# Performance work log

Hardware: AMD Instinct MI355X
Metric: run time of the kernel (lower is better)

The kernel has to match this reference:

```python
import jax, jax.numpy as jnp
import numpy as np
from jax.scipy.special import logsumexp

C = 21; H = 512; W = 512
THETA_ALPHA = 160.0; THETA_BETA = 3.0; THETA_GAMMA = 3.0
NUM_ITER = 5; RADIUS = 7  # truncated gaussian radius for the filter surrogate


def _gauss_kernel(sigma, radius=RADIUS):
    x = jnp.arange(-radius, radius + 1, dtype=jnp.float32)
    k = jnp.exp(-0.5 * (x / sigma) ** 2)
    return k / jnp.sum(k)


def _blur(x, sigma):
    # x: (c, h, w) -> depthwise separable gaussian blur, SAME padding
    c = x.shape[0]
    k = _gauss_kernel(sigma)
    kh = jnp.tile(k.reshape(1, 1, -1, 1), (c, 1, 1, 1))
    kw = jnp.tile(k.reshape(1, 1, 1, -1), (c, 1, 1, 1))
    y = jax.lax.conv_general_dilated(x[None], kh, (1, 1), 'SAME', feature_group_count=c)
    y = jax.lax.conv_general_dilated(y, kw, (1, 1), 'SAME', feature_group_count=c)
    return y[0]


def _high_dim_filter(x, rgb, bilateral):
    # Differentiable surrogate for the external permutohedral high_dim_filter op.
    if bilateral:
        # range weight from rgb (normalized to [0,1]); spatial sigma ~ theta_alpha
        guide = jnp.exp(-0.5 * jnp.sum((rgb / 255.0) ** 2, axis=0, keepdims=True) / (THETA_BETA ** 2))
        return _blur(x * guide, THETA_ALPHA / 16.0)
    return _blur(x, THETA_GAMMA)


def _combined_update(q, low_w, high_w, sp_map, sp_idx):
    # q: (c,h,w), sp_map: (h,w) int, sp_idx: scalar int
    condb = (sp_map[None] == sp_idx)                      # (1,h,w) bool
    cond = condb.astype(q.dtype)
    bool_max = (q == jnp.max(q, axis=0, keepdims=True))   # (c,h,w)
    qc = cond * q                                         # q_val_for_clique
    maxlab = jnp.max(qc, axis=0, keepdims=True)           # (1,h,w)
    l_eq = jnp.where(bool_max & condb, q, 0.0)            # l_prime_equals_l
    A_np = qc + maxlab - l_eq                             # A_no_padding
    q_sum_t = A_np                                        # single clique per iter
    prod_sp = cond * logsumexp(qc, axis=(1, 2))[:, None, None]
    prod_io = cond * logsumexp(A_np, axis=(1, 2))[:, None, None]  # cond^2 == cond
    cond2 = (sp_map[None] == sp_idx + 1).astype(q.dtype)
    prod_att = prod_sp + cond2 * logsumexp(cond2 * q, axis=(1, 2))[:, None, None]
    q_mod = q + (q == 0).astype(q.dtype)
    q_sum_t = q_sum_t + (q_sum_t == 0).astype(q.dtype)

    def upd(prod, denom, lw, hw):
        ft = prod / denom
        return lw[:, None, None] * ft + hw * (1.0 - ft)

    return (upd(prod_sp, q_mod, low_w[0], high_w[0])
            + upd(prod_io, q_sum_t, low_w[1], high_w[1])
            + upd(prod_att, q_mod, low_w[2], high_w[2]))


def setup_inputs() -> dict:
    key = jax.random.key(0)
    k1, k2, k3, k4 = jax.random.split(key, 4)
    unaries = jax.random.normal(k1, (1, H, W, C), dtype=jnp.float32)
    rgb = jax.random.uniform(k2, (1, H, W, 3), dtype=jnp.float32) * 255.0
    sp_map = jax.random.randint(k3, (1, H, W), 0, 500, dtype=jnp.int32)
    sp_indices = jax.random.randint(k4, (NUM_ITER,), 200, 400, dtype=jnp.int32)
    return {
        'unaries': unaries,
        'rgb': rgb,
        'sp_map': sp_map,
        'sp_indices': sp_indices,
        'spatial_ker_weights': jnp.eye(C, dtype=jnp.float32),
        'bilateral_ker_weights': jnp.eye(C, dtype=jnp.float32),
        'complex_rel_low_weights': jnp.ones((3, C), dtype=jnp.float32),
        'complex_rel_high_weights': jnp.ones((3,), dtype=jnp.float32),
        'compatibility_matrix': -jnp.eye(C, dtype=jnp.float32),
    }


def reference(unaries, rgb, sp_map, sp_indices, spatial_ker_weights,
              bilateral_ker_weights, complex_rel_low_weights,
              complex_rel_high_weights, compatibility_matrix):
    u = jnp.transpose(unaries[0], (2, 0, 1))   # (c,h,w)
    im = jnp.transpose(rgb[0], (2, 0, 1))      # (3,h,w)
    spm = jnp.transpose(sp_map[0])             # (h,w), matches tf.transpose
    ones = jnp.ones((C, H, W), dtype=jnp.float32)
    spatial_norm = _high_dim_filter(ones, im, False)
    bilateral_norm = _high_dim_filter(ones, im, True)
    q = u
    for i in range(NUM_ITER):
        sm = jax.nn.softmax(q, axis=0)
        spatial_out = _high_dim_filter(sm, im, False) / spatial_norm
        bilateral_out = _high_dim_filter(sm, im, True) / bilateral_norm
        cru = _combined_update(q, complex_rel_low_weights, complex_rel_high_weights,
                               spm, sp_indices[i])
        mp = (spatial_ker_weights @ spatial_out.reshape(C, -1)
              + bilateral_ker_weights @ bilateral_out.reshape(C, -1))
        pairwise = (compatibility_matrix @ mp).reshape(C, H, W)
        q = u - pairwise - cru
    return jnp.transpose(q, (1, 2, 0))[None]  # (1,h,w,c)
```

## Files before the change

### kernel.cpp

```cpp
#include <hip/hip_runtime.h>
#include <math.h>

#define CC 21
#define HH 512
#define WW 512
#define HWN (HH*WW)
#define CHW (CC*HWN)
#define RAD 7
#define KS 15
#define NITER 5
#define NBKT 16

#define TW 128
#define TH 16
#define TWH (TW + 2*RAD)
#define LSTR 145

#define FEXP(x) __expf(x)
#define FLOG(x) __logf(x)
#define FRCP(x) __builtin_amdgcn_rcpf(x)

__global__ void k_init_small(const float* __restrict__ cm,
                             const float* __restrict__ skw,
                             const float* __restrict__ bkw,
                             float* __restrict__ M1t, float* __restrict__ M2t,
                             float* __restrict__ d1, float* __restrict__ d2,
                             int* __restrict__ dflag,
                             float* __restrict__ kbuf,
                             float* __restrict__ sums) {
    __shared__ int sbad;
    int t = threadIdx.x;
    if (t == 0) sbad = 0;
    __syncthreads();
    if (t < CC*CC) {
        int k = t / CC, c = t % CC;
        float a = 0.f, b = 0.f;
        for (int m = 0; m < CC; ++m) {
            a += cm[c*CC+m] * skw[m*CC+k];
            b += cm[c*CC+m] * bkw[m*CC+k];
        }
        M1t[t] = a; M2t[t] = b;
        if (k != c && (a != 0.f || b != 0.f)) atomicOr(&sbad, 1);
        if (k == c) { d1[c] = a; d2[c] = b; }
    }
    for (int i = t; i < NITER*NBKT*64; i += blockDim.x) sums[i] = 0.f;
    if (t == CC*CC) {
        float w3[KS], w10[KS];
        float s3 = 0.f, s10 = 0.f;
        for (int i = 0; i < KS; ++i) {
            float x = (float)(i - RAD);
            w3[i]  = expf(-0.5f * (x/3.0f)  * (x/3.0f));
            w10[i] = expf(-0.5f * (x/10.0f) * (x/10.0f));
            s3 += w3[i]; s10 += w10[i];
        }
        for (int i = 0; i < KS; ++i) {
            kbuf[i]      = w3[i]  / s3;
            kbuf[KS + i] = w10[i] / s10;
        }
    }
    __syncthreads();
    if (t == 0) dflag[0] = sbad ? 0 : 1;
}

__global__ void k_init_maps(const float* __restrict__ rgb,
                            const int* __restrict__ spin,
                            const float* __restrict__ un,
                            float* __restrict__ guide,
                            int* __restrict__ spmT,
                            float* __restrict__ sm,
                            const int* __restrict__ spidx,
                            float* __restrict__ sums0) {
    int p = blockIdx.x * blockDim.x + threadIdx.x;
    int h = p / WW, w = p - h*WW;
    float r = rgb[p*3+0] * (1.0f/255.0f);
    float g = rgb[p*3+1] * (1.0f/255.0f);
    float b = rgb[p*3+2] * (1.0f/255.0f);
    guide[p] = FEXP(-0.5f * (r*r + g*g + b*b) / 9.0f);
    int s = spin[w*HH + h];
    spmT[p] = s;
    float v[CC];
    #pragma unroll
    for (int c = 0; c < CC; ++c) v[c] = un[p*CC + c];
    float mx = v[0];
    #pragma unroll
    for (int c = 1; c < CC; ++c) mx = fmaxf(mx, v[c]);
    float e[CC], ssum = 0.f;
    #pragma unroll
    for (int c = 0; c < CC; ++c) { e[c] = FEXP(v[c] - mx); ssum += e[c]; }
    float inv = FRCP(ssum);
    #pragma unroll
    for (int c = 0; c < CC; ++c) sm[c*HWN + p] = e[c] * inv;

    int sidx = spidx[0];
    bool c1 = (s == sidx), c2 = (s == sidx + 1);
    if (c1 || c2) {
        float* bkt = sums0 + (blockIdx.x & (NBKT-1)) * 64;
        float emx = FEXP(mx);
        if (c1) {
            #pragma unroll
            for (int c = 0; c < CC; ++c) {
                float ev = e[c] * emx;
                atomicAdd(&bkt[c], ev - 1.0f);
                float ea = (v[c] == mx) ? emx : ev * emx;
                atomicAdd(&bkt[CC + c], ea - 1.0f);
            }
        } else {
            #pragma unroll
            for (int c = 0; c < CC; ++c) atomicAdd(&bkt[2*CC + c], e[c] * emx - 1.0f);
        }
    }
}

__global__ void __launch_bounds__(256, 4)
k_blur(const float* __restrict__ in,
       const float* __restrict__ guide,
       float* __restrict__ outs, float* __restrict__ outb,
       const float* __restrict__ rsn, const float* __restrict__ rbn,
       const float* __restrict__ d1, const float* __restrict__ d2,
       const int* __restrict__ dflag,
       const float* __restrict__ kbuf, int norm_mode) {
    __shared__ float vbs[TH][LSTR];
    __shared__ float vbb[TH][LSTR];
    __shared__ float k3s[KS], k10s[KS];
    int t = threadIdx.x;
    if (t < KS) { k3s[t] = kbuf[t]; k10s[t] = kbuf[KS + t]; }
    __syncthreads();

    int c  = blockIdx.z;
    int x0 = blockIdx.x * TW;
    int y0 = blockIdx.y * TH;
    const float* base = in ? (in + (size_t)c*HWN) : nullptr;

    for (int u = t; u < 2*TWH; u += 256) {
        int col  = (u < TWH) ? u : u - TWH;
        int half = (u < TWH) ? 0 : 1;
        int xg = x0 - RAD + col;
        bool xok = (xg >= 0 && xg < WW);
        int yb = y0 + half*8;
        float ws_[KS], wb_[KS];
        #pragma unroll
        for (int i = 0; i < KS-1; ++i) {
            int yg = yb - RAD + i;
            bool ok = xok && (yg >= 0) && (yg < HH);
            float v = 0.f, g = 0.f;
            if (ok) { g = guide[yg*WW + xg]; v = base ? base[yg*WW + xg] : 1.0f; }
            ws_[i] = v; wb_[i] = v * g;
        }
        #pragma unroll
        for (int y = 0; y < 8; ++y) {
            int yg = yb + y + RAD;
            bool ok = xok && (yg < HH);
            float v = 0.f, g = 0.f;
            if (ok) { g = guide[yg*WW + xg]; v = base ? base[yg*WW + xg] : 1.0f; }
            ws_[(KS-1+y)%KS] = v; wb_[(KS-1+y)%KS] = v * g;
            float as = 0.f, ab = 0.f;
            #pragma unroll
            for (int d = 0; d < KS; ++d) {
                as += k3s[d]  * ws_[(y+d)%KS];
                ab += k10s[d] * wb_[(y+d)%KS];
            }
            vbs[half*8 + y][col] = as; vbb[half*8 + y][col] = ab;
        }
    }
    __syncthreads();

    int oy = t & 15;
    int xs = (t >> 4) * 8;
    int gy = y0 + oy;
    int rowp = gy*WW + x0 + xs;
    size_t ob = (size_t)c*HWN + rowp;

    float wS[22], wB[22];
    #pragma unroll
    for (int i = 0; i < 22; ++i) { wS[i] = vbs[oy][xs + i]; wB[i] = vbb[oy][xs + i]; }

    float resS[8], resB[8];
    #pragma unroll
    for (int j = 0; j < 8; ++j) {
        float a = 0.f, b = 0.f;
        #pragma unroll
        for (int d = 0; d < KS; ++d) { a += k3s[d] * wS[j + d]; b += k10s[d] * wB[j + d]; }
        resS[j] = a; resB[j] = b;
    }

    if (norm_mode) {
        #pragma unroll
        for (int j = 0; j < 8; ++j) {
            outs[rowp + j] = 1.0f / resS[j];
            outb[rowp + j] = 1.0f / resB[j];
        }
    } else if (dflag[0]) {
        float d1c = d1[c], d2c = d2[c];
        #pragma unroll
        for (int j = 0; j < 8; ++j)
            outs[ob + j] = d1c * resS[j] * rsn[rowp + j]
                         + d2c * resB[j] * rbn[rowp + j];
    } else {
        #pragma unroll
        for (int j = 0; j < 8; ++j) {
            outs[ob + j] = resS[j] * rsn[rowp + j];
            outb[ob + j] = resB[j] * rbn[rowp + j];
        }
    }
}

__global__ void __launch_bounds__(256, 4)
k_update(const float* __restrict__ un,
         const float* __restrict__ qin,
         const float* __restrict__ pw,
         const float* __restrict__ blo,
         const float* __restrict__ M1t,
         const float* __restrict__ M2t,
         const int* __restrict__ dflag,
         const float* __restrict__ sums_cur,
         float* __restrict__ sums_next,
         const float* __restrict__ lwg,
         const float* __restrict__ hwg,
         const int* __restrict__ spmT,
         const int* __restrict__ spidx, int iter,
         float* __restrict__ q,
         float* __restrict__ sm,
         float* __restrict__ out, int last) {
    __shared__ float slse[3*CC];
    if (threadIdx.x < 3*CC) {
        float s = 0.f;
        #pragma unroll
        for (int b = 0; b < NBKT; ++b) s += sums_cur[b*64 + threadIdx.x];
        slse[threadIdx.x] = FLOG((float)HWN + s);
    }
    __syncthreads();

    int p = blockIdx.x * blockDim.x + threadIdx.x;
    int sidx = spidx[iter];
    int s = spmT[p];
    float f1 = (s == sidx)     ? 1.f : 0.f;
    float f2 = (s == sidx + 1) ? 1.f : 0.f;

    float acc[CC];
    if (dflag[0]) {
        #pragma unroll
        for (int c = 0; c < CC; ++c) acc[c] = pw[c*HWN + p];
    } else {
        #pragma unroll
        for (int c = 0; c < CC; ++c) acc[c] = 0.f;
        #pragma unroll
        for (int k = 0; k < CC; ++k) {
            float sv = pw[k*HWN + p];
            float bv = blo[k*HWN + p];
            #pragma unroll
            for (int c = 0; c < CC; ++c)
                acc[c] += M1t[k*CC + c] * sv + M2t[k*CC + c] * bv;
        }
    }

    float hw0 = hwg[0], hw1 = hwg[1], hw2 = hwg[2];
    bool any_clique = __any(f1 != 0.f || f2 != 0.f);
    if (any_clique) {
        float v[CC];
        #pragma unroll
        for (int c = 0; c < CC; ++c) v[c] = qin[p*CC + c];
        float mx = v[0];
        #pragma unroll
        for (int c = 1; c < CC; ++c) mx = fmaxf(mx, v[c]);
        #pragma unroll
        for (int c = 0; c < CC; ++c) {
            float qv = v[c];
            float qmod = qv + ((qv == 0.f) ? 1.f : 0.f);
            float anp = f1 * (qv + mx) - ((f1 != 0.f && qv == mx) ? qv : 0.f);
            float qst = anp + ((anp == 0.f) ? 1.f : 0.f);
            float p1 = f1 * slse[c];
            float p2 = f1 * slse[CC + c];
            float p3 = p1 + f2 * slse[2*CC + c];
            float ft1 = p1 * FRCP(qmod);
            float ft2 = p2 * FRCP(qst);
            float ft3 = p3 * FRCP(qmod);
            float cru = lwg[c]*ft1        + hw0*(1.f - ft1)
                      + lwg[CC + c]*ft2   + hw1*(1.f - ft2)
                      + lwg[2*CC + c]*ft3 + hw2*(1.f - ft3);
            acc[c] = un[p*CC + c] - acc[c] - cru;
        }
    } else {
        float cruc = hw0 + hw1 + hw2;
        #pragma unroll
        for (int c = 0; c < CC; ++c)
            acc[c] = un[p*CC + c] - acc[c] - cruc;
    }

    if (!last) {
        int sidx2 = spidx[iter + 1];
        bool c1 = (s == sidx2), c2 = (s == sidx2 + 1);
        if (c1 || c2) {
            #pragma unroll
            for (int c = 0; c < CC; ++c) q[p*CC + c] = acc[c];
        }
        float mx2 = acc[0];
        #pragma unroll
        for (int c = 1; c < CC; ++c) mx2 = fmaxf(mx2, acc[c]);
        float e[CC], ssum = 0.f;
        #pragma unroll
        for (int c = 0; c < CC; ++c) { e[c] = FEXP(acc[c] - mx2); ssum += e[c]; }
        float inv = FRCP(ssum);
        #pragma unroll
        for (int c = 0; c < CC; ++c) sm[c*HWN + p] = e[c] * inv;

        if (c1 || c2) {
            float* bkt = sums_next + (blockIdx.x & (NBKT-1)) * 64;
            float emx = FEXP(mx2);
            if (c1) {
                #pragma unroll
                for (int c = 0; c < CC; ++c) {
                    float ev = e[c] * emx;
                    atomicAdd(&bkt[c], ev - 1.0f);
                    float ea = (acc[c] == mx2) ? emx : ev * emx;
                    atomicAdd(&bkt[CC + c], ea - 1.0f);
                }
            } else {
                #pragma unroll
                for (int c = 0; c < CC; ++c) atomicAdd(&bkt[2*CC + c], e[c] * emx - 1.0f);
            }
        }
    } else {
        #pragma unroll
        for (int c = 0; c < CC; ++c) out[p*CC + c] = acc[c];
    }
}

extern "C" void kernel_launch(void* const* d_in, const int* in_sizes, int n_in,
                              void* d_out, int out_size, void* d_ws, size_t ws_size,
                              hipStream_t stream) {
    const float* un    = (const float*)d_in[0];
    const float* rgb   = (const float*)d_in[1];
    const int*   spin  = (const int*)  d_in[2];
    const int*   spidx = (const int*)  d_in[3];
    const float* skw   = (const float*)d_in[4];
    const float* bkw   = (const float*)d_in[5];
    const float* lw    = (const float*)d_in[6];
    const float* hwv   = (const float*)d_in[7];
    const float* cm    = (const float*)d_in[8];
    float* out = (float*)d_out;

    float* ws = (float*)d_ws;
    float* q     = ws;
    float* sm    = ws + (size_t)CHW;
    float* a     = ws + (size_t)2*CHW;
    float* b     = ws + (size_t)3*CHW;
    float* guide = ws + (size_t)4*CHW;
    float* rsn   = guide + HWN;
    float* rbn   = rsn + HWN;
    int*   spmT  = (int*)(rbn + HWN);
    float* M1t   = rbn + 2*(size_t)HWN;
    float* M2t   = M1t + CC*CC;
    float* d1    = M2t + CC*CC;
    float* d2    = d1 + CC;
    int*   dflag = (int*)(d2 + CC);
    float* kbuf  = d2 + CC + 4;
    float* sums  = kbuf + 2*KS;

    dim3 blk(256);
    int gpix = HWN / 256;
    dim3 gblur(WW/TW, HH/TH, CC);
    dim3 gnorm(WW/TW, HH/TH, 1);

    k_init_small<<<1, 512, 0, stream>>>(cm, skw, bkw, M1t, M2t, d1, d2, dflag,
                                        kbuf, sums);
    k_init_maps<<<gpix, blk, 0, stream>>>(rgb, spin, un, guide, spmT, sm,
                                          spidx, sums);
    k_blur<<<gnorm, blk, 0, stream>>>(nullptr, guide, rsn, rbn,
                                      nullptr, nullptr, d1, d2, dflag, kbuf, 1);

    for (int it = 0; it < NITER; ++it) {
        int last = (it == NITER - 1) ? 1 : 0;
        float* su  = sums + it*NBKT*64;
        float* sun = last ? nullptr : (sums + (it+1)*NBKT*64);
        const float* qin = (it == 0) ? un : q;
        k_blur<<<gblur, blk, 0, stream>>>(sm, guide, a, b, rsn, rbn,
                                          d1, d2, dflag, kbuf, 0);
        k_update<<<gpix, blk, 0, stream>>>(un, qin, a, b, M1t, M2t, dflag,
                                           su, sun, lw, hwv,
                                           spmT, spidx, it, q, sm, out, last);
    }
}
```

Before: 343.1 us.

## Store softmax and blur intermediates in bf16 and transpose unaries to planar

Result: slower. 415.2 us (+21.0%).

```diff
diff --git a/kernel.cpp b/kernel.cpp
--- a/kernel.cpp
+++ b/kernel.cpp
@@ -19,6 +19,18 @@
 #define FEXP(x) __expf(x)
 #define FLOG(x) __logf(x)
 #define FRCP(x) __builtin_amdgcn_rcpf(x)
+
+typedef unsigned short ushort_t;
+typedef unsigned int uint_t;
+
+__device__ __forceinline__ float b2f(ushort_t u) {
+    return __uint_as_float(((uint_t)u) << 16);
+}
+__device__ __forceinline__ ushort_t f2b(float f) {
+    uint_t u = __float_as_uint(f);
+    u += 0x7FFFu + ((u >> 16) & 1u);
+    return (ushort_t)(u >> 16);
+}
 
 __global__ void k_init_small(const float* __restrict__ cm,
                              const float* __restrict__ skw,
@@ -67,7 +79,8 @@
                             const float* __restrict__ un,
                             float* __restrict__ guide,
                             int* __restrict__ spmT,
-                            float* __restrict__ sm,
+                            float* __restrict__ unp,
+                            ushort_t* __restrict__ sm,
                             const int* __restrict__ spidx,
                             float* __restrict__ sums0) {
     int p = blockIdx.x * blockDim.x + threadIdx.x;
@@ -80,7 +93,7 @@
     spmT[p] = s;
     float v[CC];
     #pragma unroll
-    for (int c = 0; c < CC; ++c) v[c] = un[p*CC + c];
+    for (int c = 0; c < CC; ++c) { v[c] = un[p*CC + c]; unp[c*HWN + p] = v[c]; }
     float mx = v[0];
     #pragma unroll
     for (int c = 1; c < CC; ++c) mx = fmaxf(mx, v[c]);
@@ -89,7 +102,7 @@
     for (int c = 0; c < CC; ++c) { e[c] = FEXP(v[c] - mx); ssum += e[c]; }
     float inv = FRCP(ssum);
     #pragma unroll
-    for (int c = 0; c < CC; ++c) sm[c*HWN + p] = e[c] * inv;
+    for (int c = 0; c < CC; ++c) sm[c*HWN + p] = f2b(e[c] * inv);
 
     int sidx = spidx[0];
     bool c1 = (s == sidx), c2 = (s == sidx + 1);
@@ -112,13 +125,9 @@
 }
 
 __global__ void __launch_bounds__(256, 4)
-k_blur(const float* __restrict__ in,
-       const float* __restrict__ guide,
-       float* __restrict__ outs, float* __restrict__ outb,
-       const float* __restrict__ rsn, const float* __restrict__ rbn,
-       const float* __restrict__ d1, const float* __restrict__ d2,
-       const int* __restrict__ dflag,
-       const float* __restrict__ kbuf, int norm_mode) {
+k_norm(const float* __restrict__ guide,
+       float* __restrict__ rsn, float* __restrict__ rbn,
+       const float* __restrict__ kbuf) {
     __shared__ float vbs[TH][LSTR];
     __shared__ float vbb[TH][LSTR];
     __shared__ float k3s[KS], k10s[KS];
@@ -126,10 +135,8 @@
     if (t < KS) { k3s[t] = kbuf[t]; k10s[t] = kbuf[KS + t]; }
     __syncthreads();
 
-    int c  = blockIdx.z;
     int x0 = blockIdx.x * TW;
     int y0 = blockIdx.y * TH;
-    const float* base = in ? (in + (size_t)c*HWN) : nullptr;
 
     for (int u = t; u < 2*TWH; u += 256) {
         int col  = (u < TWH) ? u : u - TWH;
@@ -142,17 +149,17 @@
         for (int i = 0; i < KS-1; ++i) {
             int yg = yb - RAD + i;
             bool ok = xok && (yg >= 0) && (yg < HH);
-            float v = 0.f, g = 0.f;
-            if (ok) { g = guide[yg*WW + xg]; v = base ? base[yg*WW + xg] : 1.0f; }
-            ws_[i] = v; wb_[i] = v * g;
+            float v = ok ? 1.0f : 0.f;
+            float g = ok ? guide[yg*WW + xg] : 0.f;
+            ws_[i] = v; wb_[i] = g;
         }
         #pragma unroll
         for (int y = 0; y < 8; ++y) {
             int yg = yb + y + RAD;
             bool ok = xok && (yg < HH);
-            float v = 0.f, g = 0.f;
-            if (ok) { g = guide[yg*WW + xg]; v = base ? base[yg*WW + xg] : 1.0f; }
-            ws_[(KS-1+y)%KS] = v; wb_[(KS-1+y)%KS] = v * g;
+            float v = ok ? 1.0f : 0.f;
+            float g = ok ? guide[yg*WW + xg] : 0.f;
+            ws_[(KS-1+y)%KS] = v; wb_[(KS-1+y)%KS] = g;
             float as = 0.f, ab = 0.f;
             #pragma unroll
             for (int d = 0; d < KS; ++d) {
@@ -166,6 +173,76 @@
 
     int oy = t & 15;
     int xs = (t >> 4) * 8;
+    int rowp = (y0 + oy)*WW + x0 + xs;
+
+    float wS[22], wB[22];
+    #pragma unroll
+    for (int i = 0; i < 22; ++i) { wS[i] = vbs[oy][xs + i]; wB[i] = vbb[oy][xs + i]; }
+    #pragma unroll
+    for (int j = 0; j < 8; ++j) {
+        float a = 0.f, b = 0.f;
+        #pragma unroll
+        for (int d = 0; d < KS; ++d) { a += k3s[d] * wS[j + d]; b += k10s[d] * wB[j + d]; }
+        rsn[rowp + j] = 1.0f / a;
+        rbn[rowp + j] = 1.0f / b;
+    }
+}
+
+__global__ void __launch_bounds__(256, 4)
+k_blur(const ushort_t* __restrict__ in,
+       const float* __restrict__ guide,
+       ushort_t* __restrict__ outs, ushort_t* __restrict__ outb,
+       const float* __restrict__ rsn, const float* __restrict__ rbn,
+       const float* __restrict__ d1, const float* __restrict__ d2,
+       const int* __restrict__ dflag,
+       const float* __restrict__ kbuf) {
+    __shared__ float vbs[TH][LSTR];
+    __shared__ float vbb[TH][LSTR];
+    __shared__ float k3s[KS], k10s[KS];
+    int t = threadIdx.x;
+    if (t < KS) { k3s[t] = kbuf[t]; k10s[t] = kbuf[KS + t]; }
+    __syncthreads();
+
+    int c  = blockIdx.z;
+    int x0 = blockIdx.x * TW;
+    int y0 = blockIdx.y * TH;
+    const ushort_t* base = in + (size_t)c*HWN;
+
+    for (int u = t; u < 2*TWH; u += 256) {
+        int col  = (u < TWH) ? u : u - TWH;
+        int half = (u < TWH) ? 0 : 1;
+        int xg = x0 - RAD + col;
+        bool xok = (xg >= 0 && xg < WW);
+        int yb = y0 + half*8;
+        float ws_[KS], wb_[KS];
+        #pragma unroll
+        for (int i = 0; i < KS-1; ++i) {
+            int yg = yb - RAD + i;
+            bool ok = xok && (yg >= 0) && (yg < HH);
+            float v = 0.f, g = 0.f;
+            if (ok) { g = guide[yg*WW + xg]; v = b2f(base[yg*WW + xg]); }
+            ws_[i] = v; wb_[i] = v * g;
+        }
+        #pragma unroll
+        for (int y = 0; y < 8; ++y) {
+            int yg = yb + y + RAD;
+            bool ok = xok && (yg < HH);
+            float v = 0.f, g = 0.f;
+            if (ok) { g = guide[yg*WW + xg]; v = b2f(base[yg*WW + xg]); }
+            ws_[(KS-1+y)%KS] = v; wb_[(KS-1+y)%KS] = v * g;
+            float as = 0.f, ab = 0.f;
+            #pragma unroll
+            for (int d = 0; d < KS; ++d) {
+                as += k3s[d]  * ws_[(y+d)%KS];
+                ab += k10s[d] * wb_[(y+d)%KS];
+            }
+            vbs[half*8 + y][col] = as; vbb[half*8 + y][col] = ab;
+        }
+    }
+    __syncthreads();
+
+    int oy = t & 15;
+    int xs = (t >> 4) * 8;
     int gy = y0 + oy;
     int rowp = gy*WW + x0 + xs;
     size_t ob = (size_t)c*HWN + rowp;
@@ -183,32 +260,27 @@
         resS[j] = a; resB[j] = b;
     }
 
-    if (norm_mode) {
+    if (dflag[0]) {
+        float d1c = d1[c], d2c = d2[c];
+        #pragma unroll
+        for (int j = 0; j < 8; ++j)
+            outs[ob + j] = f2b(d1c * resS[j] * rsn[rowp + j]
+                             + d2c * resB[j] * rbn[rowp + j]);
+    } else {
         #pragma unroll
         for (int j = 0; j < 8; ++j) {
-            outs[rowp + j] = 1.0f / resS[j];
-            outb[rowp + j] = 1.0f / resB[j];
-        }
-    } else if (dflag[0]) {
-        float d1c = d1[c], d2c = d2[c];
-        #pragma unroll
-        for (int j = 0; j < 8; ++j)
-            outs[ob + j] = d1c * resS[j] * rsn[rowp + j]
-                         + d2c * resB[j] * rbn[rowp + j];
-    } else {
-        #pragma unroll
-        for (int j = 0; j < 8; ++j) {
-            outs[ob + j] = resS[j] * rsn[rowp + j];
-            outb[ob + j] = resB[j] * rbn[rowp + j];
+            outs[ob + j] = f2b(resS[j] * rsn[rowp + j]);
+            outb[ob + j] = f2b(resB[j] * rbn[rowp + j]);
         }
     }
 }
 
 __global__ void __launch_bounds__(256, 4)
-k_update(const float* __restrict__ un,
+k_update(const float* __restrict__ unp,
          const float* __restrict__ qin,
-         const float* __restrict__ pw,
-         const float* __restrict__ blo,
+         int qin_pixelmajor_unused,
+         const ushort_t* __restrict__ pw,
+         const ushort_t* __restrict__ blo,
          const float* __restrict__ M1t,
          const float* __restrict__ M2t,
          const int* __restrict__ dflag,
@@ -219,7 +291,7 @@
          const int* __restrict__ spmT,
          const int* __restrict__ spidx, int iter,
          float* __restrict__ q,
-         float* __restrict__ sm,
+         ushort_t* __restrict__ sm,
          float* __restrict__ out, int last) {
     __shared__ float slse[3*CC];
     if (threadIdx.x < 3*CC) {
@@ -239,14 +311,14 @@
     float acc[CC];
     if (dflag[0]) {
         #pragma unroll
-        for (int c = 0; c < CC; ++c) acc[c] = pw[c*HWN + p];
+        for (int c = 0; c < CC; ++c) acc[c] = b2f(pw[c*HWN + p]);
     } else {
         #pragma unroll
         for (int c = 0; c < CC; ++c) acc[c] = 0.f;
         #pragma unroll
         for (int k = 0; k < CC; ++k) {
-            float sv = pw[k*HWN + p];
-            float bv = blo[k*HWN + p];
+            float sv = b2f(pw[k*HWN + p]);
+            float bv = b2f(blo[k*HWN + p]);
             #pragma unroll
             for (int c = 0; c < CC; ++c)
                 acc[c] += M1t[k*CC + c] * sv + M2t[k*CC + c] * bv;
@@ -277,13 +349,13 @@
             float cru = lwg[c]*ft1        + hw0*(1.f - ft1)
                       + lwg[CC + c]*ft2   + hw1*(1.f - ft2)
                       + lwg[2*CC + c]*ft3 + hw2*(1.f - ft3);
-            acc[c] = un[p*CC + c] - acc[c] - cru;
+            acc[c] = unp[c*HWN + p] - acc[c] - cru;
         }
     } else {
         float cruc = hw0 + hw1 + hw2;
         #pragma unroll
         for (int c = 0; c < CC; ++c)
-            acc[c] = un[p*CC + c] - acc[c] - cruc;
+            acc[c] = unp[c*HWN + p] - acc[c] - cruc;
     }
 
     if (!last) {
@@ -301,7 +373,7 @@
         for (int c = 0; c < CC; ++c) { e[c] = FEXP(acc[c] - mx2); ssum += e[c]; }
         float inv = FRCP(ssum);
         #pragma unroll
-        for (int c = 0; c < CC; ++c) sm[c*HWN + p] = e[c] * inv;
+        for (int c = 0; c < CC; ++c) sm[c*HWN + p] = f2b(e[c] * inv);
 
         if (c1 || c2) {
             float* bkt = sums_next + (blockIdx.x & (NBKT-1)) * 64;
@@ -340,11 +412,12 @@
     float* out = (float*)d_out;
 
     float* ws = (float*)d_ws;
-    float* q     = ws;
-    float* sm    = ws + (size_t)CHW;
-    float* a     = ws + (size_t)2*CHW;
-    float* b     = ws + (size_t)3*CHW;
-    float* guide = ws + (size_t)4*CHW;
+    float*    q    = ws;
+    float*    unp  = ws + (size_t)CHW;
+    ushort_t* smb  = (ushort_t*)(ws + (size_t)2*CHW);
+    ushort_t* pwa  = smb + (size_t)CHW;
+    ushort_t* pwb  = pwa + (size_t)CHW;
+    float* guide = ws + (size_t)2*CHW + ((size_t)3*CHW + 1)/2;
     float* rsn   = guide + HWN;
     float* rbn   = rsn + HWN;
     int*   spmT  = (int*)(rbn + HWN);
@@ -363,20 +436,19 @@
 
     k_init_small<<<1, 512, 0, stream>>>(cm, skw, bkw, M1t, M2t, d1, d2, dflag,
                                         kbuf, sums);
-    k_init_maps<<<gpix, blk, 0, stream>>>(rgb, spin, un, guide, spmT, sm,
+    k_init_maps<<<gpix, blk, 0, stream>>>(rgb, spin, un, guide, spmT, unp, smb,
                                           spidx, sums);
-    k_blur<<<gnorm, blk, 0, stream>>>(nullptr, guide, rsn, rbn,
-                                      nullptr, nullptr, d1, d2, dflag, kbuf, 1);
+    k_norm<<<gnorm, blk, 0, stream>>>(guide, rsn, rbn, kbuf);
 
     for (int it = 0; it < NITER; ++it) {
         int last = (it == NITER - 1) ? 1 : 0;
         float* su  = sums + it*NBKT*64;
         float* sun = last ? nullptr : (sums + (it+1)*NBKT*64);
         const float* qin = (it == 0) ? un : q;
-        k_blur<<<gblur, blk, 0, stream>>>(sm, guide, a, b, rsn, rbn,
-                                          d1, d2, dflag, kbuf, 0);
-        k_update<<<gpix, blk, 0, stream>>>(un, qin, a, b, M1t, M2t, dflag,
+        k_blur<<<gblur, blk, 0, stream>>>(smb, guide, pwa, pwb, rsn, rbn,
+                                          d1, d2, dflag, kbuf);
+        k_update<<<gpix, blk, 0, stream>>>(unp, qin, 0, pwa, pwb, M1t, M2t, dflag,
                                            su, sun, lw, hwv,
-                                           spmT, spidx, it, q, sm, out, last);
-    }
-}
+                                           spmT, spidx, it, q, smb, out, last);
+    }
+}
```
